# Optimization experiments

Hardware: AMD Instinct MI355X
Metric: run time of the kernel (lower is better)

The kernel has to match this reference:

```python
import jax, jax.numpy as jnp
import numpy as np

B, S, H = 1, 2048, 2048
NH, KVH, D = 32, 8, 64
G = NH // KVH  # num_key_value_groups = 4


def setup_inputs() -> dict:
    key = jax.random.key(0)
    k1, k2, k3 = jax.random.split(key, 3)
    x = jax.random.normal(k1, (B, S, H), dtype=jnp.float32)
    w_qkv = jax.random.normal(k2, ((NH + 2 * KVH) * D, H), dtype=jnp.float32) * 0.02
    w_o = jax.random.normal(k3, (H, NH * D), dtype=jnp.float32) * 0.02
    return {"x": x, "w_qkv": w_qkv, "w_o": w_o}


def _rope_cos_sin(seqlen, dim, dtype):
    inv_freq = 1.0 / (10000.0 ** (jnp.arange(0, dim, 2, dtype=jnp.float32) / dim))
    t = jnp.arange(seqlen, dtype=jnp.float32)
    freqs = jnp.outer(t, inv_freq)  # [S, D/2]
    return jnp.cos(freqs).astype(dtype), jnp.sin(freqs).astype(dtype)


def _apply_rope(x, cos, sin):
    # x: [B,S,h,D]; non-interleaved half rotation (flash-attn RotaryEmbedding)
    d2 = x.shape[-1] // 2
    x1, x2 = x[..., :d2], x[..., d2:]
    c = cos[None, :, None, :]
    s = sin[None, :, None, :]
    return jnp.concatenate([x1 * c - x2 * s, x2 * c + x1 * s], axis=-1)


def reference(x, w_qkv, w_o):
    b, s, _ = x.shape
    qkv = x @ w_qkv.T  # fused QKV proj: [B,S,(NH+2*KVH)*D]
    q, kv = jnp.split(qkv, [NH * D], axis=-1)
    q = q.reshape(b, s, NH, D)
    kv = kv.reshape(b, s, 2, KVH, D)
    cos, sin = _rope_cos_sin(s, D, x.dtype)
    q = _apply_rope(q, cos, sin)
    k = _apply_rope(kv[:, :, 0], cos, sin)
    v = kv[:, :, 1]
    # GQA: group q heads per kv head instead of repeat_interleave (same math)
    qg = q.reshape(b, s, KVH, G, D)
    scale = 1.0 / np.sqrt(D).astype(np.float32)
    scores = jnp.einsum('bskgd,btkd->bkgst', qg, k) * scale  # [B,KVH,G,S,S]
    causal = jnp.tril(jnp.ones((s, s), dtype=bool))
    scores = jnp.where(causal[None, None, None], scores, jnp.asarray(-jnp.inf, scores.dtype))
    p = jax.nn.softmax(scores, axis=-1)
    out = jnp.einsum('bkgst,btkd->bskgd', p, v).reshape(b, s, NH * D)
    return out @ w_o.T
```

## Files before the change

### kernel.cpp

```cpp
#include <hip/hip_runtime.h>


typedef __bf16 bf16_t;
typedef __attribute__((ext_vector_type(8))) __bf16 bf16x8;
typedef __attribute__((ext_vector_type(4))) __bf16 bf16x4;
typedef __attribute__((ext_vector_type(4))) float f32x4;

#define S_LEN 2048
#define H_DIM 2048
#define NHEAD 32
#define KVH 8
#define HD 64
#define QKV_N 3072

#define ENT_STRIDE 8320

__global__ void cast3_kernel(const float* __restrict__ x, const float* __restrict__ wq,
                             const float* __restrict__ wo, bf16_t* __restrict__ xb,
                             bf16_t* __restrict__ wqb, bf16_t* __restrict__ wob) {
  int i = blockIdx.x * blockDim.x + threadIdx.x;
  const int n1 = S_LEN * H_DIM / 4, n2 = QKV_N * H_DIM / 4, n3 = H_DIM * H_DIM / 4;
  const float* src; bf16_t* dst; int j;
  if (i < n1)           { src = x;  dst = xb;  j = i; }
  else if (i < n1 + n2) { src = wq; dst = wqb; j = i - n1; }
  else if (i < n1 + n2 + n3) { src = wo; dst = wob; j = i - n1 - n2; }
  else return;
  float4 v = ((const float4*)src)[j];
  bf16x4 o;
  o.x = (bf16_t)v.x; o.y = (bf16_t)v.y; o.z = (bf16_t)v.z; o.w = (bf16_t)v.w;
  ((bf16x4*)dst)[j] = o;
}

__device__ __forceinline__ void async_copy16(bf16_t* lds_base, const bf16_t* g) {
  __builtin_amdgcn_global_load_lds(
      (const __attribute__((address_space(1))) unsigned int*)g,
      (__attribute__((address_space(3))) unsigned int*)lds_base, 16, 0, 0);
}

#define TBM 128
#define TBN 128
#define TBK 32

__global__ __launch_bounds__(256) void gemm128(const bf16_t* __restrict__ A,
                                               const bf16_t* __restrict__ B,
                                               float* __restrict__ C,
                                               int M, int N, int K) {
  __shared__ __align__(16) bf16_t As[3][TBM * TBK];
  __shared__ __align__(16) bf16_t Bs[3][TBM * TBK];

  const int tid  = threadIdx.x;
  const int lane = tid & 63;
  const int w    = tid >> 6;
  const int wm   = (w >> 1) * 64;
  const int wn   = (w & 1) * 64;
  const int c    = lane & 15;
  const int quad = lane >> 4;
  const int m0   = blockIdx.y * TBM;
  const int n0   = blockIdx.x * TBN;

  f32x4 acc[4][4] = {};

  const bf16_t* Ab = A + (size_t)m0 * K;
  const bf16_t* Bb = B + (size_t)n0 * K;

  int srow[2], skch[2], sbase[2];
#pragma unroll
  for (int i = 0; i < 2; ++i) {
    int chunkbase = i * 256 + w * 64;
    int chunk = chunkbase + lane;
    sbase[i] = chunkbase * 8;
    srow[i]  = chunk >> 2;
    skch[i]  = (chunk & 3) ^ ((chunk >> 3) & 3);
  }

  auto stage = [&](int buf, int k0) {
#pragma unroll
    for (int i = 0; i < 2; ++i) {
      const bf16_t* ga = Ab + (size_t)srow[i] * K + k0 + skch[i] * 8;
      const bf16_t* gb = Bb + (size_t)srow[i] * K + k0 + skch[i] * 8;
      async_copy16(&As[buf][sbase[i]], ga);
      async_copy16(&Bs[buf][sbase[i]], gb);
    }
  };

  auto compute = [&](int buf) {
    bf16x8 af[4], bfr[4];
#pragma unroll
    for (int mt = 0; mt < 4; ++mt) {
      int row = wm + mt * 16 + c;
      int kch = quad ^ ((row >> 1) & 3);
      af[mt] = *(const bf16x8*)&As[buf][(row * 4 + kch) * 8];
    }
#pragma unroll
    for (int nt = 0; nt < 4; ++nt) {
      int rowb = wn + nt * 16 + c;
      int kch = quad ^ ((rowb >> 1) & 3);
      bfr[nt] = *(const bf16x8*)&Bs[buf][(rowb * 4 + kch) * 8];
    }
#pragma unroll
    for (int mt = 0; mt < 4; ++mt)
#pragma unroll
      for (int nt = 0; nt < 4; ++nt)
        acc[mt][nt] = __builtin_amdgcn_mfma_f32_16x16x32_bf16(af[mt], bfr[nt], acc[mt][nt], 0, 0, 0);
  };

  const int NS = K / TBK;
  stage(0, 0);
  stage(1, TBK);
  int sc = 0, sp = 2;
  for (int k = 0; k < NS; ++k) {
    if (k + 1 < NS) {
      asm volatile("s_waitcnt vmcnt(4)" ::: "memory");
    } else {
      asm volatile("s_waitcnt vmcnt(0)" ::: "memory");
    }
    __builtin_amdgcn_s_barrier();
    if (k + 2 < NS) stage(sp, (k + 2) * TBK);
    compute(sc);
    sc = (sc == 2) ? 0 : sc + 1;
    sp = (sp == 2) ? 0 : sp + 1;
  }

#pragma unroll
  for (int mt = 0; mt < 4; ++mt)
#pragma unroll
    for (int nt = 0; nt < 4; ++nt)
#pragma unroll
      for (int reg = 0; reg < 4; ++reg) {
        int row = m0 + wm + mt * 16 + quad * 4 + reg;
        int col = n0 + wn + nt * 16 + c;
        C[(size_t)row * N + col] = acc[mt][nt][reg];
      }
}

__global__ void rope_kernel(const float* __restrict__ qkv,
                            bf16_t* __restrict__ qb,
                            bf16_t* __restrict__ kt,
                            bf16_t* __restrict__ vt) {
  const int s = blockIdx.x;
  const float* row = qkv + (size_t)s * QKV_N;
  for (int idx = threadIdx.x; idx < (NHEAD + KVH) * 32; idx += blockDim.x) {
    int h = idx >> 5;
    int i = idx & 31;
    float inv = __expf(-(float)i * (9.210340371976184f / 32.0f));
    float ang = (float)s * inv;
    float c, sn;
    __sincosf(ang, &sn, &c);
    if (h < NHEAD) {
      const float* base = row + h * HD;
      float x1 = base[i], x2 = base[i + 32];
      float o1 = (x1 * c - x2 * sn) * 0.125f;
      float o2 = (x2 * c + x1 * sn) * 0.125f;
      bf16_t* q = qb + (size_t)s * H_DIM + h * HD;
      q[i] = (bf16_t)o1;
      q[i + 32] = (bf16_t)o2;
    } else {
      int kh = h - NHEAD;
      const float* base = row + H_DIM + kh * HD;
      float x1 = base[i], x2 = base[i + 32];
      float o1 = x1 * c - x2 * sn;
      float o2 = x2 * c + x1 * sn;
      bf16_t* k = kt + ((size_t)kh * S_LEN + s) * HD;
      k[i] = (bf16_t)o1;
      k[i + 32] = (bf16_t)o2;
    }
  }
  for (int j = threadIdx.x; j < KVH * HD; j += blockDim.x) {
    int kh = j >> 6, d = j & 63;
    vt[((size_t)kh * S_LEN + s) * HD + d] = (bf16_t)row[H_DIM + KVH * HD + kh * HD + d];
  }
}

__global__ __launch_bounds__(256) void vtrans_kernel(const bf16_t* __restrict__ vt,
                                                     bf16_t* __restrict__ vt2) {
  __shared__ bf16_t L[64 * 65];
  const int kh = blockIdx.x;
  const int t0 = blockIdx.y * 64;
#pragma unroll
  for (int it = 0; it < 2; ++it) {
    int idx = it * 256 + threadIdx.x;
    int srow = idx >> 3, doff = (idx & 7) * 8;
    bf16x8 v = *(const bf16x8*)(vt + ((size_t)kh * S_LEN + t0 + srow) * HD + doff);
#pragma unroll
    for (int j = 0; j < 8; ++j) L[(doff + j) * 65 + srow] = v[j];
  }
  __syncthreads();
  int d = threadIdx.x >> 2, soff = (threadIdx.x & 3) * 16;
  bf16x8 o0, o1;
#pragma unroll
  for (int j = 0; j < 8; ++j) o0[j] = L[d * 65 + soff + j];
#pragma unroll
  for (int j = 0; j < 8; ++j) o1[j] = L[d * 65 + soff + 8 + j];
  *(bf16x8*)(vt2 + ((size_t)kh * HD + d) * S_LEN + t0 + soff) = o0;
  *(bf16x8*)(vt2 + ((size_t)kh * HD + d) * S_LEN + t0 + soff + 8) = o1;
}

#define PSTR 72

__global__ __launch_bounds__(256) void flash_split(const bf16_t* __restrict__ qb,
                                                   const bf16_t* __restrict__ kt,
                                                   const bf16_t* __restrict__ vt2,
                                                   float* __restrict__ pbuf,
                                                   bf16_t* __restrict__ attn) {
  __shared__ __align__(16) bf16_t Ks[64 * 64];
  __shared__ __align__(16) bf16_t Vs[64 * 64];
  __shared__ __align__(16) bf16_t Ps[4][32 * PSTR];

  const int tid  = threadIdx.x;
  const int lane = tid & 63;
  const int w    = tid >> 6;
  const int e    = (int)gridDim.x - 1 - (int)blockIdx.x;
  const int kh   = e / 160;
  const int i    = e - kh * 160;

  int qt, t_begin, t_end;
  {
    int T;
    if (i < 16)      { qt = i;                T = (qt >> 1) + 1; t_begin = 0;                 t_end = T; }
    else if (i < 48) { int r = i - 16; qt = 16 + (r >> 1); int ck = r & 1;
                       T = (qt >> 1) + 1; t_begin = (ck * T) >> 1;      t_end = ((ck + 1) * T) >> 1; }
    else if (i < 96) { int r = i - 48; qt = 32 + r / 3;    int ck = r % 3;
                       T = (qt >> 1) + 1; t_begin = (ck * T) / 3;       t_end = ((ck + 1) * T) / 3; }
    else             { int r = i - 96; qt = 48 + (r >> 2); int ck = r & 3;
                       T = (qt >> 1) + 1; t_begin = (ck * T) >> 2;      t_end = ((ck + 1) * T) >> 2; }
  }
  const int T     = (qt >> 1) + 1;
  const int s0    = qt * 32;
  const int h     = kh * 4 + w;
  const int c     = lane & 15;
  const int quad  = lane >> 4;

  bf16x8 qf[2][2];
#pragma unroll
  for (int rf = 0; rf < 2; ++rf)
#pragma unroll
    for (int ks = 0; ks < 2; ++ks)
      qf[rf][ks] = *(const bf16x8*)(qb + (size_t)(s0 + rf * 16 + c) * H_DIM + h * HD + ks * 32 + quad * 8);

  f32x4 acc[2][4] = {};
  float lsum[2] = {0.f, 0.f};

  const bf16_t* kbase = kt + (size_t)kh * S_LEN * HD;
  const bf16_t* vbase = vt2 + (size_t)kh * HD * S_LEN;

  int srow[2], skc[2], sbase[2];
#pragma unroll
  for (int i2 = 0; i2 < 2; ++i2) {
    int chunkbase = i2 * 256 + w * 64;
    int p = chunkbase + lane;
    sbase[i2] = chunkbase * 8;
    srow[i2]  = p >> 3;
    skc[i2]   = (p & 7) ^ (srow[i2] & 7);
  }

  for (int tile = t_begin; tile < t_end; ++tile) {
    const int t0 = tile * 64;
    __syncthreads();
#pragma unroll
    for (int i2 = 0; i2 < 2; ++i2) {
      async_copy16(&Ks[sbase[i2]], kbase + (size_t)(t0 + srow[i2]) * HD + skc[i2] * 8);
      async_copy16(&Vs[sbase[i2]], vbase + (size_t)srow[i2] * S_LEN + t0 + skc[i2] * 8);
    }
    __syncthreads();

    const bool masked = (tile == T - 1);
    int nact = 4;
    if (masked) { nact = ((s0 + 31 - t0) >> 4) + 1; if (nact > 4) nact = 4; }
    const int nkh = (nact + 1) >> 1;

#pragma unroll
    for (int rf = 0; rf < 2; ++rf) {
      for (int kt2 = 0; kt2 < nact; ++kt2) {
        f32x4 st = {};
#pragma unroll
        for (int ks = 0; ks < 2; ++ks) {
          bf16x8 kf = *(const bf16x8*)&Ks[((kt2 * 16 + c) * 8 + ((ks * 4 + quad) ^ (c & 7))) * 8];
          st = __builtin_amdgcn_mfma_f32_16x16x32_bf16(kf, qf[rf][ks], st, 0, 0, 0);
        }
        const int row = s0 + rf * 16 + c;
        bf16x4 pk;
#pragma unroll
        for (int reg = 0; reg < 4; ++reg) {
          const int key = t0 + kt2 * 16 + quad * 4 + reg;
          float p = __expf(st[reg] - 8.0f);
          if (masked && key > row) p = 0.f;
          pk[reg] = (bf16_t)p;
          lsum[rf] += p;
        }
        *(bf16x4*)&Ps[w][(rf * 16 + c) * PSTR + kt2 * 16 + quad * 4] = pk;
      }
      for (int kt2 = nact; kt2 < 2 * nkh; ++kt2) {
        bf16x4 z = {};
        *(bf16x4*)&Ps[w][(rf * 16 + c) * PSTR + kt2 * 16 + quad * 4] = z;
      }
    }

    for (int kh2 = 0; kh2 < nkh; ++kh2) {
      bf16x8 vf[4];
#pragma unroll
      for (int dt = 0; dt < 4; ++dt)
        vf[dt] = *(const bf16x8*)&Vs[((dt * 16 + c) * 8 + ((kh2 * 4 + quad) ^ (c & 7))) * 8];
#pragma unroll
      for (int rf = 0; rf < 2; ++rf) {
        bf16x8 pa = *(const bf16x8*)&Ps[w][(rf * 16 + c) * PSTR + kh2 * 32 + quad * 8];
#pragma unroll
        for (int dt = 0; dt < 4; ++dt)
          acc[rf][dt] = __builtin_amdgcn_mfma_f32_16x16x32_bf16(pa, vf[dt], acc[rf][dt], 0, 0, 0);
      }
    }
  }

#pragma unroll
  for (int rf = 0; rf < 2; ++rf) {
    lsum[rf] += __shfl_xor(lsum[rf], 16);
    lsum[rf] += __shfl_xor(lsum[rf], 32);
  }

  if (i < 16) {
    float* lbuf = (float*)&Ps[w][0];
#pragma unroll
    for (int rf = 0; rf < 2; ++rf) lbuf[rf * 16 + c] = lsum[rf];
    asm volatile("s_waitcnt lgkmcnt(0)" ::: "memory");
#pragma unroll
    for (int rf = 0; rf < 2; ++rf)
#pragma unroll
      for (int reg = 0; reg < 4; ++reg) {
        const float inv = 1.0f / lbuf[rf * 16 + quad * 4 + reg];
        const int row = s0 + rf * 16 + quad * 4 + reg;
#pragma unroll
        for (int dt = 0; dt < 4; ++dt)
          attn[(size_t)row * H_DIM + h * HD + dt * 16 + c] = (bf16_t)(acc[rf][dt][reg] * inv);
      }
  } else {
    float* ent = pbuf + (size_t)e * ENT_STRIDE;
#pragma unroll
    for (int rf = 0; rf < 2; ++rf) {
#pragma unroll
      for (int dt = 0; dt < 4; ++dt)
#pragma unroll
        for (int reg = 0; reg < 4; ++reg)
          ent[w * 2048 + (rf * 16 + quad * 4 + reg) * 64 + dt * 16 + c] = acc[rf][dt][reg];
      ent[8192 + w * 32 + rf * 16 + c] = lsum[rf];
    }
  }
}

__global__ __launch_bounds__(256) void flash_reduce(const float* __restrict__ pbuf,
                                                    bf16_t* __restrict__ attn) {
  const int kh = blockIdx.x / 48;
  const int qt = 16 + (blockIdx.x % 48);
  const int b  = qt >> 4;
  int base;
  if (b == 1)      base = kh * 160 + 16 + (qt - 16) * 2;
  else if (b == 2) base = kh * 160 + 48 + (qt - 32) * 3;
  else             base = kh * 160 + 96 + (qt - 48) * 4;
  const int nch = b + 1;

  const int t   = threadIdx.x;
  const int h2  = t >> 6;
  const int row = (t >> 1) & 31;
  const int dh  = t & 1;

  f32x4 o[8] = {};
  float l = 0.f;
  for (int ci = 0; ci < nch; ++ci) {
    const float* ent = pbuf + (size_t)(base + ci) * ENT_STRIDE;
    const float* p = ent + h2 * 2048 + row * 64 + dh * 32;
#pragma unroll
    for (int j = 0; j < 8; ++j) {
      f32x4 v = ((const f32x4*)p)[j];
      o[j][0] += v[0]; o[j][1] += v[1]; o[j][2] += v[2]; o[j][3] += v[3];
    }
    l += ent[8192 + h2 * 32 + row];
  }
  const float inv = 1.0f / l;
  bf16_t* dst = attn + (size_t)(qt * 32 + row) * H_DIM + (kh * 4 + h2) * 64 + dh * 32;
#pragma unroll
  for (int j = 0; j < 8; ++j) {
    bf16x4 ov;
    ov[0] = (bf16_t)(o[j][0] * inv); ov[1] = (bf16_t)(o[j][1] * inv);
    ov[2] = (bf16_t)(o[j][2] * inv); ov[3] = (bf16_t)(o[j][3] * inv);
    *(bf16x4*)(dst + j * 4) = ov;
  }
}

extern "C" void kernel_launch(void* const* d_in, const int* in_sizes, int n_in,
                              void* d_out, int out_size, void* d_ws, size_t ws_size,
                              hipStream_t stream) {
  const float* x     = (const float*)d_in[0];
  const float* w_qkv = (const float*)d_in[1];
  const float* w_o   = (const float*)d_in[2];
  float* out = (float*)d_out;

  char* ws = (char*)d_ws;
  size_t off = 0;
  bf16_t* x_bf    = (bf16_t*)(ws + off); off += (size_t)S_LEN * H_DIM * 2;
  bf16_t* wqkv_bf = (bf16_t*)(ws + off); off += (size_t)QKV_N * H_DIM * 2;
  float*  qkv     = (float*) (ws + off); off += (size_t)S_LEN * QKV_N * 4;
  float*  pbuf    = (float*)ws;
  bf16_t* wo_bf   = (bf16_t*)(ws + off); off += (size_t)H_DIM * H_DIM * 2;
  bf16_t* q_bf    = (bf16_t*)(ws + off); off += (size_t)S_LEN * H_DIM * 2;
  bf16_t* k_t     = (bf16_t*)(ws + off); off += (size_t)KVH * S_LEN * HD * 2;
  bf16_t* v_t     = (bf16_t*)(ws + off); off += (size_t)KVH * S_LEN * HD * 2;
  bf16_t* v_t2    = (bf16_t*)(ws + off); off += (size_t)KVH * S_LEN * HD * 2;
  bf16_t* attn    = (bf16_t*)(ws + off); off += (size_t)S_LEN * H_DIM * 2;

  const int ntot = (S_LEN * H_DIM + QKV_N * H_DIM + H_DIM * H_DIM) / 4;
  cast3_kernel<<<(ntot + 255) / 256, 256, 0, stream>>>(x, w_qkv, w_o, x_bf, wqkv_bf, wo_bf);

  gemm128<<<dim3(QKV_N / TBN, S_LEN / TBM), 256, 0, stream>>>(x_bf, wqkv_bf, qkv, S_LEN, QKV_N, H_DIM);

  rope_kernel<<<S_LEN, 256, 0, stream>>>(qkv, q_bf, k_t, v_t);

  vtrans_kernel<<<dim3(KVH, S_LEN / 64), 256, 0, stream>>>(v_t, v_t2);

  flash_split<<<1280, 256, 0, stream>>>(q_bf, k_t, v_t2, pbuf, attn);
  flash_reduce<<<384, 256, 0, stream>>>(pbuf, attn);

  gemm128<<<dim3(H_DIM / TBN, S_LEN / TBM), 256, 0, stream>>>(attn, wo_bf, out, S_LEN, H_DIM, H_DIM);
}
```

Before: 246.8 us.

## Fuse RoPE and V transpose into QKV GEMM epilogue, use 512-thread GEMM

Moves the RoPE rotation, Q scaling, K layout and V transpose into the epilogue of the QKV projection GEMM. This removes the fp32 qkv intermediate and two separate kernels (rope and vtrans). The GEMM now runs 512 threads per block, each warp covering a 32x64 sub-tile. The workspace is overlaid so the flash partial buffer reuses the region that held the bf16 x and weights. The epilogue does scattered 2-byte stores and recomputes sincos per element, and smaller per-warp tiles lower MFMA reuse per LDS load.

```diff
diff --git a/kernel.cpp b/kernel.cpp
--- a/kernel.cpp
+++ b/kernel.cpp
@@ -37,56 +37,49 @@
       (__attribute__((address_space(3))) unsigned int*)lds_base, 16, 0, 0);
 }
 
-#define TBM 128
-#define TBN 128
-#define TBK 32
-
-__global__ __launch_bounds__(256) void gemm128(const bf16_t* __restrict__ A,
+#define GBM 128
+#define GBN 128
+#define GBK 32
+
+template <int EPI>
+__global__ __launch_bounds__(512) void gemm512(const bf16_t* __restrict__ A,
                                                const bf16_t* __restrict__ B,
                                                float* __restrict__ C,
+                                               bf16_t* __restrict__ qb,
+                                               bf16_t* __restrict__ ktp,
+                                               bf16_t* __restrict__ vt2,
                                                int M, int N, int K) {
-  __shared__ __align__(16) bf16_t As[3][TBM * TBK];
-  __shared__ __align__(16) bf16_t Bs[3][TBM * TBK];
+  __shared__ __align__(16) bf16_t As[3][GBM * GBK];
+  __shared__ __align__(16) bf16_t Bs[3][GBM * GBK];
 
   const int tid  = threadIdx.x;
   const int lane = tid & 63;
   const int w    = tid >> 6;
-  const int wm   = (w >> 1) * 64;
+  const int wm   = (w >> 1) * 32;
   const int wn   = (w & 1) * 64;
   const int c    = lane & 15;
   const int quad = lane >> 4;
-  const int m0   = blockIdx.y * TBM;
-  const int n0   = blockIdx.x * TBN;
-
-  f32x4 acc[4][4] = {};
+  const int m0   = blockIdx.y * GBM;
+  const int n0   = blockIdx.x * GBN;
+
+  f32x4 acc[2][4] = {};
 
   const bf16_t* Ab = A + (size_t)m0 * K;
   const bf16_t* Bb = B + (size_t)n0 * K;
 
-  int srow[2], skch[2], sbase[2];
-#pragma unroll
-  for (int i = 0; i < 2; ++i) {
-    int chunkbase = i * 256 + w * 64;
-    int chunk = chunkbase + lane;
-    sbase[i] = chunkbase * 8;
-    srow[i]  = chunk >> 2;
-    skch[i]  = (chunk & 3) ^ ((chunk >> 3) & 3);
-  }
+  const int srow = tid >> 2;
+  const int skch = (tid & 3) ^ ((tid >> 3) & 3);
+  const int sbase = (w * 64) * 8;
 
   auto stage = [&](int buf, int k0) {
-#pragma unroll
-    for (int i = 0; i < 2; ++i) {
-      const bf16_t* ga = Ab + (size_t)srow[i] * K + k0 + skch[i] * 8;
-      const bf16_t* gb = Bb + (size_t)srow[i] * K + k0 + skch[i] * 8;
-      async_copy16(&As[buf][sbase[i]], ga);
-      async_copy16(&Bs[buf][sbase[i]], gb);
-    }
+    async_copy16(&As[buf][sbase], Ab + (size_t)srow * K + k0 + skch * 8);
+    async_copy16(&Bs[buf][sbase], Bb + (size_t)srow * K + k0 + skch * 8);
   };
 
   auto compute = [&](int buf) {
-    bf16x8 af[4], bfr[4];
-#pragma unroll
-    for (int mt = 0; mt < 4; ++mt) {
+    bf16x8 af[2], bfr[4];
+#pragma unroll
+    for (int mt = 0; mt < 2; ++mt) {
       int row = wm + mt * 16 + c;
       int kch = quad ^ ((row >> 1) & 3);
       af[mt] = *(const bf16x8*)&As[buf][(row * 4 + kch) * 8];
@@ -98,101 +91,96 @@
       bfr[nt] = *(const bf16x8*)&Bs[buf][(rowb * 4 + kch) * 8];
     }
 #pragma unroll
-    for (int mt = 0; mt < 4; ++mt)
+    for (int mt = 0; mt < 2; ++mt)
 #pragma unroll
       for (int nt = 0; nt < 4; ++nt)
         acc[mt][nt] = __builtin_amdgcn_mfma_f32_16x16x32_bf16(af[mt], bfr[nt], acc[mt][nt], 0, 0, 0);
   };
 
-  const int NS = K / TBK;
+  const int NS = K / GBK;
   stage(0, 0);
-  stage(1, TBK);
+  stage(1, GBK);
   int sc = 0, sp = 2;
   for (int k = 0; k < NS; ++k) {
     if (k + 1 < NS) {
-      asm volatile("s_waitcnt vmcnt(4)" ::: "memory");
+      asm volatile("s_waitcnt vmcnt(2)" ::: "memory");
     } else {
       asm volatile("s_waitcnt vmcnt(0)" ::: "memory");
     }
     __builtin_amdgcn_s_barrier();
-    if (k + 2 < NS) stage(sp, (k + 2) * TBK);
+    if (k + 2 < NS) stage(sp, (k + 2) * GBK);
     compute(sc);
     sc = (sc == 2) ? 0 : sc + 1;
     sp = (sp == 2) ? 0 : sp + 1;
   }
 
-#pragma unroll
-  for (int mt = 0; mt < 4; ++mt)
-#pragma unroll
-    for (int nt = 0; nt < 4; ++nt)
-#pragma unroll
-      for (int reg = 0; reg < 4; ++reg) {
-        int row = m0 + wm + mt * 16 + quad * 4 + reg;
-        int col = n0 + wn + nt * 16 + c;
-        C[(size_t)row * N + col] = acc[mt][nt][reg];
-      }
-}
-
-__global__ void rope_kernel(const float* __restrict__ qkv,
-                            bf16_t* __restrict__ qb,
-                            bf16_t* __restrict__ kt,
-                            bf16_t* __restrict__ vt) {
-  const int s = blockIdx.x;
-  const float* row = qkv + (size_t)s * QKV_N;
-  for (int idx = threadIdx.x; idx < (NHEAD + KVH) * 32; idx += blockDim.x) {
-    int h = idx >> 5;
-    int i = idx & 31;
-    float inv = __expf(-(float)i * (9.210340371976184f / 32.0f));
-    float ang = (float)s * inv;
-    float c, sn;
-    __sincosf(ang, &sn, &c);
-    if (h < NHEAD) {
-      const float* base = row + h * HD;
-      float x1 = base[i], x2 = base[i + 32];
-      float o1 = (x1 * c - x2 * sn) * 0.125f;
-      float o2 = (x2 * c + x1 * sn) * 0.125f;
-      bf16_t* q = qb + (size_t)s * H_DIM + h * HD;
-      q[i] = (bf16_t)o1;
-      q[i + 32] = (bf16_t)o2;
+  if (EPI == 0) {
+#pragma unroll
+    for (int mt = 0; mt < 2; ++mt)
+#pragma unroll
+      for (int nt = 0; nt < 4; ++nt)
+#pragma unroll
+        for (int reg = 0; reg < 4; ++reg) {
+          int row = m0 + wm + mt * 16 + quad * 4 + reg;
+          int col = n0 + wn + nt * 16 + c;
+          C[(size_t)row * N + col] = acc[mt][nt][reg];
+        }
+  } else {
+    const int colb = n0 + wn;
+    if (colb < NHEAD * HD) {
+      const int h = colb >> 6;
+#pragma unroll
+      for (int nt = 0; nt < 2; ++nt) {
+        const int i = nt * 16 + c;
+        const float invf = __expf(-(float)i * (9.210340371976184f / 32.0f));
+#pragma unroll
+        for (int mt = 0; mt < 2; ++mt)
+#pragma unroll
+          for (int reg = 0; reg < 4; ++reg) {
+            const int s = m0 + wm + mt * 16 + quad * 4 + reg;
+            float sn, cs;
+            __sincosf((float)s * invf, &sn, &cs);
+            const float x1 = acc[mt][nt][reg], x2 = acc[mt][nt + 2][reg];
+            bf16_t* q = qb + (size_t)s * H_DIM + h * HD;
+            q[i]      = (bf16_t)((x1 * cs - x2 * sn) * 0.125f);
+            q[i + 32] = (bf16_t)((x2 * cs + x1 * sn) * 0.125f);
+          }
+      }
+    } else if (colb < NHEAD * HD + KVH * HD) {
+      const int kh = (colb - NHEAD * HD) >> 6;
+#pragma unroll
+      for (int nt = 0; nt < 2; ++nt) {
+        const int i = nt * 16 + c;
+        const float invf = __expf(-(float)i * (9.210340371976184f / 32.0f));
+#pragma unroll
+        for (int mt = 0; mt < 2; ++mt)
+#pragma unroll
+          for (int reg = 0; reg < 4; ++reg) {
+            const int s = m0 + wm + mt * 16 + quad * 4 + reg;
+            float sn, cs;
+            __sincosf((float)s * invf, &sn, &cs);
+            const float x1 = acc[mt][nt][reg], x2 = acc[mt][nt + 2][reg];
+            bf16_t* kd = ktp + ((size_t)kh * S_LEN + s) * HD;
+            kd[i]      = (bf16_t)(x1 * cs - x2 * sn);
+            kd[i + 32] = (bf16_t)(x2 * cs + x1 * sn);
+          }
+      }
     } else {
-      int kh = h - NHEAD;
-      const float* base = row + H_DIM + kh * HD;
-      float x1 = base[i], x2 = base[i + 32];
-      float o1 = x1 * c - x2 * sn;
-      float o2 = x2 * c + x1 * sn;
-      bf16_t* k = kt + ((size_t)kh * S_LEN + s) * HD;
-      k[i] = (bf16_t)o1;
-      k[i + 32] = (bf16_t)o2;
-    }
-  }
-  for (int j = threadIdx.x; j < KVH * HD; j += blockDim.x) {
-    int kh = j >> 6, d = j & 63;
-    vt[((size_t)kh * S_LEN + s) * HD + d] = (bf16_t)row[H_DIM + KVH * HD + kh * HD + d];
-  }
-}
-
-__global__ __launch_bounds__(256) void vtrans_kernel(const bf16_t* __restrict__ vt,
-                                                     bf16_t* __restrict__ vt2) {
-  __shared__ bf16_t L[64 * 65];
-  const int kh = blockIdx.x;
-  const int t0 = blockIdx.y * 64;
-#pragma unroll
-  for (int it = 0; it < 2; ++it) {
-    int idx = it * 256 + threadIdx.x;
-    int srow = idx >> 3, doff = (idx & 7) * 8;
-    bf16x8 v = *(const bf16x8*)(vt + ((size_t)kh * S_LEN + t0 + srow) * HD + doff);
-#pragma unroll
-    for (int j = 0; j < 8; ++j) L[(doff + j) * 65 + srow] = v[j];
-  }
-  __syncthreads();
-  int d = threadIdx.x >> 2, soff = (threadIdx.x & 3) * 16;
-  bf16x8 o0, o1;
-#pragma unroll
-  for (int j = 0; j < 8; ++j) o0[j] = L[d * 65 + soff + j];
-#pragma unroll
-  for (int j = 0; j < 8; ++j) o1[j] = L[d * 65 + soff + 8 + j];
-  *(bf16x8*)(vt2 + ((size_t)kh * HD + d) * S_LEN + t0 + soff) = o0;
-  *(bf16x8*)(vt2 + ((size_t)kh * HD + d) * S_LEN + t0 + soff + 8) = o1;
+      const int kh = (colb - NHEAD * HD - KVH * HD) >> 6;
+#pragma unroll
+      for (int nt = 0; nt < 4; ++nt) {
+        const int d = nt * 16 + c;
+#pragma unroll
+        for (int mt = 0; mt < 2; ++mt) {
+          const int sr = m0 + wm + mt * 16 + quad * 4;
+          bf16x4 pv;
+#pragma unroll
+          for (int reg = 0; reg < 4; ++reg) pv[reg] = (bf16_t)acc[mt][nt][reg];
+          *(bf16x4*)&vt2[((size_t)kh * HD + d) * S_LEN + sr] = pv;
+        }
+      }
+    }
+  }
 }
 
 #define PSTR 72
@@ -393,29 +381,26 @@
   float* out = (float*)d_out;
 
   char* ws = (char*)d_ws;
-  size_t off = 0;
-  bf16_t* x_bf    = (bf16_t*)(ws + off); off += (size_t)S_LEN * H_DIM * 2;
-  bf16_t* wqkv_bf = (bf16_t*)(ws + off); off += (size_t)QKV_N * H_DIM * 2;
-  float*  qkv     = (float*) (ws + off); off += (size_t)S_LEN * QKV_N * 4;
+  const size_t OVERLAY = (size_t)1280 * ENT_STRIDE * 4;
+  bf16_t* x_bf    = (bf16_t*)ws;
+  bf16_t* wqkv_bf = (bf16_t*)(ws + (size_t)S_LEN * H_DIM * 2);
   float*  pbuf    = (float*)ws;
+  size_t off = OVERLAY;
   bf16_t* wo_bf   = (bf16_t*)(ws + off); off += (size_t)H_DIM * H_DIM * 2;
   bf16_t* q_bf    = (bf16_t*)(ws + off); off += (size_t)S_LEN * H_DIM * 2;
   bf16_t* k_t     = (bf16_t*)(ws + off); off += (size_t)KVH * S_LEN * HD * 2;
-  bf16_t* v_t     = (bf16_t*)(ws + off); off += (size_t)KVH * S_LEN * HD * 2;
   bf16_t* v_t2    = (bf16_t*)(ws + off); off += (size_t)KVH * S_LEN * HD * 2;
   bf16_t* attn    = (bf16_t*)(ws + off); off += (size_t)S_LEN * H_DIM * 2;
 
   const int ntot = (S_LEN * H_DIM + QKV_N * H_DIM + H_DIM * H_DIM) / 4;
   cast3_kernel<<<(ntot + 255) / 256, 256, 0, stream>>>(x, w_qkv, w_o, x_bf, wqkv_bf, wo_bf);
 
-  gemm128<<<dim3(QKV_N / TBN, S_LEN / TBM), 256, 0, stream>>>(x_bf, wqkv_bf, qkv, S_LEN, QKV_N, H_DIM);
-
-  rope_kernel<<<S_LEN, 256, 0, stream>>>(qkv, q_bf, k_t, v_t);
-
-  vtrans_kernel<<<dim3(KVH, S_LEN / 64), 256, 0, stream>>>(v_t, v_t2);
+  gemm512<1><<<dim3(QKV_N / GBN, S_LEN / GBM), 512, 0, stream>>>(
+      x_bf, wqkv_bf, nullptr, q_bf, k_t, v_t2, S_LEN, QKV_N, H_DIM);
 
   flash_split<<<1280, 256, 0, stream>>>(q_bf, k_t, v_t2, pbuf, attn);
   flash_reduce<<<384, 256, 0, stream>>>(pbuf, attn);
 
-  gemm128<<<dim3(H_DIM / TBN, S_LEN / TBM), 256, 0, stream>>>(attn, wo_bf, out, S_LEN, H_DIM, H_DIM);
-}
+  gemm512<0><<<dim3(H_DIM / GBN, S_LEN / GBM), 512, 0, stream>>>(
+      attn, wo_bf, out, nullptr, nullptr, nullptr, S_LEN, H_DIM, H_DIM);
+}
```

Result: faster. 233.3 us (-5.5%).
